# Performance work log

Hardware: AMD Instinct MI355X
Metric: run time of the kernel (lower is better)

The kernel has to match this reference:

```python
import jax, jax.numpy as jnp
import numpy as np

NEG_INF = -1e30  # stand-in for float('-inf') that is softmax-safe


def setup_inputs() -> dict:
    key = jax.random.key(0)
    ks = jax.random.split(key, 6)
    B, H, S, D = 2, 8, 1024, 64
    NF, K = 4, 3
    return {
        "query": jax.random.normal(ks[0], (B, H, S, D), dtype=jnp.float32),
        "keys": jax.random.normal(ks[1], (B, H, S, D), dtype=jnp.float32),
        "vals": jax.random.normal(ks[2], (B, H, S, D), dtype=jnp.float32),
        "mask": jnp.ones((B, 1, S, S), dtype=jnp.int32),
        "conv_w": jax.random.normal(ks[3], (NF, 1, K, K), dtype=jnp.float32) * (1.0 / K),
        "conv_b": jnp.zeros((NF,), dtype=jnp.float32),
        "lin_w": jax.random.normal(ks[4], (1, NF), dtype=jnp.float32) * 0.5,
        "lin_b": jnp.zeros((1,), dtype=jnp.float32),
    }


def reference(query, keys, vals, mask, conv_w, conv_b, lin_w, lin_b):
    B, H, S, D = query.shape
    NF = conv_w.shape[0]
    K = conv_w.shape[2]
    scale = jnp.asarray(D, query.dtype) ** 0.5

    # [B,H,S,S] raw dot-product scores
    dp = jnp.einsum("bhsd,bhtd->bhst", query, keys) / scale

    # conv2d over the score matrix: treat (B*H) as batch, 1 input channel
    x = dp.reshape(B * H, 1, S, S)
    conv = jax.lax.conv_general_dilated(
        x, conv_w,
        window_strides=(1, 1),
        padding=[(K // 2, K // 2), (K // 2, K // 2)],
        dimension_numbers=("NCHW", "OIHW", "NCHW"),
    ) + conv_b[None, :, None, None]
    conv = jax.nn.leaky_relu(conv, negative_slope=0.01)  # [B*H, NF, S, S]

    # per-pixel linear over the filter axis (Linear(num_filters, 1))
    conv = conv.reshape(B, H, NF, S, S)
    preattn = jnp.einsum("bhfst,f->bhst", conv, lin_w[0]) + lin_b[0]

    # masking + softmax (mask broadcasts over heads)
    preattn = jnp.where(mask == 0, jnp.asarray(NEG_INF, preattn.dtype), preattn)
    attn = jax.nn.softmax(preattn, axis=-1)

    # dropout is identity in eval mode
    return jnp.einsum("bhst,bhtd->bhsd", attn, vals)
```

## Files before the change

### kernel.cpp

```cpp
#include <hip/hip_runtime.h>
#include <math.h>

#define S_LEN 1024
#define D_DIM 64
#define NBH   16

typedef unsigned short ushort_t;
typedef unsigned int uint_t;
typedef __attribute__((ext_vector_type(8))) short short8;
typedef __attribute__((ext_vector_type(4))) short short4v;
typedef __attribute__((ext_vector_type(4))) float f32x4;
typedef __attribute__((ext_vector_type(2))) float f32x2;
typedef __attribute__((ext_vector_type(2))) _Float16 h2;

__device__ __forceinline__ ushort_t rne_bf16(float x) {
    unsigned u = __float_as_uint(x);
    return (ushort_t)((u + 0x7FFFu + ((u >> 16) & 1u)) >> 16);
}
__device__ __forceinline__ void split1(float x, ushort_t& h, ushort_t& l) {
    h = rne_bf16(x);
    float hf = __uint_as_float((unsigned)h << 16);
    l = rne_bf16(x - hf);
}
__device__ __forceinline__ ushort_t f16bits(float x) {
    _Float16 h = (_Float16)x;
    ushort_t b;
    __builtin_memcpy(&b, &h, 2);
    return b;
}
__device__ __forceinline__ float h2f(ushort_t b) {
    _Float16 h;
    __builtin_memcpy(&h, &b, 2);
    return (float)h;
}
__device__ __forceinline__ h2 as_h2(uint_t u) {
    h2 r;
    __builtin_memcpy(&r, &u, 4);
    return r;
}

__global__ __launch_bounds__(256) void prep(
    const float* __restrict__ k, const float* __restrict__ v,
    const int* __restrict__ mask,
    ushort_t* __restrict__ khi, ushort_t* __restrict__ klo,
    ushort_t* __restrict__ vhi, ushort_t* __restrict__ vlo,
    unsigned* __restrict__ mw)
{
    __shared__ float Ls[64][65];
    const int tid = threadIdx.x;
    const int bx = blockIdx.x;
    if (bx < 512) {
        const int gid  = bx * 256 + tid;
        const int bh   = gid >> 13;
        const int tile = (gid >> 7) & 63;
        const int ch   = (gid >> 6) & 1;
        const int lane = gid & 63;
        const int quad = lane >> 4, t15 = lane & 15;
        const float* src = k + ((size_t)bh * S_LEN + tile * 16 + t15) * D_DIM
                             + ch * 32 + quad * 8;
        float x[8];
        *(float4*)(x + 0) = *(const float4*)(src);
        *(float4*)(x + 4) = *(const float4*)(src + 4);
        short8 hv, lv;
        #pragma unroll
        for (int i = 0; i < 8; ++i) {
            ushort_t h, l;
            split1(x[i], h, l);
            hv[i] = (short)h; lv[i] = (short)l;
        }
        *(short8*)(khi + (size_t)gid * 8) = hv;
        *(short8*)(klo + (size_t)gid * 8) = lv;
    } else if (bx < 768) {
        const int bi = bx - 512;
        const int tt = bi & 15, bh = bi >> 4;
        const float* vb = v + ((size_t)bh * S_LEN + tt * 64) * D_DIM;
        #pragma unroll
        for (int p = 0; p < 4; ++p) {
            int idx = p * 1024 + tid * 4;
            int r = idx >> 6, c = idx & 63;
            float4 x = *(const float4*)(vb + r * 64 + c);
            Ls[r][c] = x.x; Ls[r][c+1] = x.y; Ls[r][c+2] = x.z; Ls[r][c+3] = x.w;
        }
        __syncthreads();
        const int d = tid >> 2, c0 = (tid & 3) * 16;
        ushort_t hi[16], lo[16];
        #pragma unroll
        for (int j = 0; j < 16; ++j) split1(Ls[c0 + j][d], hi[j], lo[j]);
        const int tb0 = tt * 8 + (c0 >> 3);
        const size_t o0 = (((size_t)bh * 128 + tb0) * 64 + d) * 8;
        const size_t o1 = (((size_t)bh * 128 + tb0 + 1) * 64 + d) * 8;
        *(short8*)(vhi + o0) = *(short8*)(hi);
        *(short8*)(vhi + o1) = *(short8*)(hi + 8);
        *(short8*)(vlo + o0) = *(short8*)(lo);
        *(short8*)(vlo + o1) = *(short8*)(lo + 8);
    } else {
        const int gid = (bx - 768) * 256 + tid;
        const int row = gid >> 5, wd = gid & 31;
        const int4* mp = (const int4*)(mask + (size_t)row * 1024 + wd * 32);
        unsigned bits = 0;
        #pragma unroll
        for (int p = 0; p < 8; ++p) {
            int4 qv = mp[p];
            bits |= (qv.x != 0 ? 1u : 0u) << (p * 4 + 0);
            bits |= (qv.y != 0 ? 1u : 0u) << (p * 4 + 1);
            bits |= (qv.z != 0 ? 1u : 0u) << (p * 4 + 2);
            bits |= (qv.w != 0 ? 1u : 0u) << (p * 4 + 3);
        }
        mw[(size_t)row * 32 + wd] = bits;
    }
}

#define DPSTR 1040
#define PSTR  1048
__global__ __launch_bounds__(512) void fused_qk_conv_av(
    const float* __restrict__ q,
    const ushort_t* __restrict__ khi, const ushort_t* __restrict__ klo,
    const unsigned* __restrict__ mw,
    const ushort_t* __restrict__ vhi, const ushort_t* __restrict__ vlo,
    const float* __restrict__ conv_w, const float* __restrict__ conv_b,
    const float* __restrict__ lin_w, const float* __restrict__ lin_b,
    float* __restrict__ out)
{
    __shared__ ushort_t dpH[18 * DPSTR];
    __shared__ ushort_t pP[16 * PSTR];
    __shared__ float oBuf[16][68];
    __shared__ float lsPart[16][4];
    __shared__ unsigned mb[16][32];

    const int st = blockIdx.x, bh = blockIdx.y;
    const int s0 = st * 16;
    const int b  = bh >> 3;
    const int tid = threadIdx.x;
    const int wave = tid >> 6, lane = tid & 63;
    const int m = lane & 15, quad = lane >> 4;

    {
        const int row = tid >> 5, wd = tid & 31;
        mb[row][wd] = mw[((size_t)b * S_LEN + s0 + row) * 32 + wd];
    }

    short8 AH0[2], AH1[2], AL0[2], AL1[2];
    #pragma unroll
    for (int set = 0; set < 2; ++set) {
        const int sA = s0 - 1 + 2 * set + m;
        const int sQ = sA < 0 ? 0 : (sA > S_LEN - 1 ? S_LEN - 1 : sA);
        const float* qp = q + ((size_t)bh * S_LEN + sQ) * D_DIM + quad * 8;
        float qa[16];
        *(float4*)(qa + 0)  = *(const float4*)(qp + 0);
        *(float4*)(qa + 4)  = *(const float4*)(qp + 4);
        *(float4*)(qa + 8)  = *(const float4*)(qp + 32);
        *(float4*)(qa + 12) = *(const float4*)(qp + 36);
        #pragma unroll
        for (int i = 0; i < 8; ++i) {
            ushort_t h, l;
            split1(qa[i] * 0.125f, h, l);
            AH0[set][i] = (short)h; AL0[set][i] = (short)l;
            split1(qa[8 + i] * 0.125f, h, l);
            AH1[set][i] = (short)h; AL1[set][i] = (short)l;
        }
    }

    #pragma unroll
    for (int tt = 0; tt < 8; ++tt) {
        const int tile = wave * 8 + tt;
        const size_t kb = (((size_t)bh * 64 + tile) * 128 + lane) * 8;
        short8 KH0 = *(const short8*)(khi + kb);
        short8 KL0 = *(const short8*)(klo + kb);
        short8 KH1 = *(const short8*)(khi + kb + 512);
        short8 KL1 = *(const short8*)(klo + kb + 512);
        const int col = tile * 16 + m;
        {
            f32x4 a0 = {0.f, 0.f, 0.f, 0.f}, a1 = {0.f, 0.f, 0.f, 0.f};
            a0 = __builtin_amdgcn_mfma_f32_16x16x32_bf16(AH0[0], KH0, a0, 0, 0, 0);
            a1 = __builtin_amdgcn_mfma_f32_16x16x32_bf16(AH1[0], KH1, a1, 0, 0, 0);
            a0 = __builtin_amdgcn_mfma_f32_16x16x32_bf16(AH0[0], KL0, a0, 0, 0, 0);
            a1 = __builtin_amdgcn_mfma_f32_16x16x32_bf16(AH1[0], KL1, a1, 0, 0, 0);
            a0 = __builtin_amdgcn_mfma_f32_16x16x32_bf16(AL0[0], KH0, a0, 0, 0, 0);
            a1 = __builtin_amdgcn_mfma_f32_16x16x32_bf16(AL1[0], KH1, a1, 0, 0, 0);
            #pragma unroll
            for (int r = 0; r < 4; ++r) {
                const int row = quad * 4 + r;
                const int s = s0 - 1 + row;
                const float v = (s >= 0 && s < S_LEN) ? a0[r] + a1[r] : 0.f;
                dpH[row * DPSTR + col] = f16bits(v);
            }
        }
        {
            f32x4 a0 = {0.f, 0.f, 0.f, 0.f}, a1 = {0.f, 0.f, 0.f, 0.f};
            a0 = __builtin_amdgcn_mfma_f32_16x16x32_bf16(AH0[1], KH0, a0, 0, 0, 0);
            a1 = __builtin_amdgcn_mfma_f32_16x16x32_bf16(AH1[1], KH1, a1, 0, 0, 0);
            a0 = __builtin_amdgcn_mfma_f32_16x16x32_bf16(AH0[1], KL0, a0, 0, 0, 0);
            a1 = __builtin_amdgcn_mfma_f32_16x16x32_bf16(AH1[1], KL1, a1, 0, 0, 0);
            a0 = __builtin_amdgcn_mfma_f32_16x16x32_bf16(AL0[1], KH0, a0, 0, 0, 0);
            a1 = __builtin_amdgcn_mfma_f32_16x16x32_bf16(AL1[1], KH1, a1, 0, 0, 0);
            if (quad == 3) {
                #pragma unroll
                for (int r = 2; r < 4; ++r) {
                    const int mrow = quad * 4 + r;
                    const int s = s0 + 1 + mrow;
                    const float v = (s < S_LEN) ? a0[r] + a1[r] : 0.f;
                    dpH[(mrow + 2) * DPSTR + col] = f16bits(v);
                }
            }
        }
    }

    float w[36];
    #pragma unroll
    for (int i = 0; i < 36; ++i) w[i] = conv_w[i];
    float cb[4], lw[4];
    #pragma unroll
    for (int f = 0; f < 4; ++f) { cb[f] = conv_b[f]; lw[f] = lin_w[f]; }
    const float lb = lin_b[0];

    __syncthreads();

    const int rh = tid >> 8, cg = tid & 255, c0 = cg * 4;
    #pragma unroll
    for (int pass = 0; pass < 2; ++pass) {
        const int obase = rh * 8 + pass * 4;
        float rowv[6][6];
        #pragma unroll
        for (int jj = 0; jj < 6; ++jj) {
            const ushort_t* rp = &dpH[(obase + jj) * DPSTR + c0];
            uint2 dd = *(const uint2*)rp;
            h2 p0 = as_h2(dd.x), p1 = as_h2(dd.y);
            rowv[jj][0] = cg ? h2f(rp[-1]) : 0.f;
            rowv[jj][1] = (float)p0[0]; rowv[jj][2] = (float)p0[1];
            rowv[jj][3] = (float)p1[0]; rowv[jj][4] = (float)p1[1];
            rowv[jj][5] = (cg < 255) ? h2f(rp[4]) : 0.f;
        }
        float ls[4];
        #pragma unroll
        for (int jo = 0; jo < 4; ++jo) {
            const int o = obase + jo;
            f32x2 pa = {lb, lb}, pb = {lb, lb};
            #pragma unroll
            for (int f = 0; f < 4; ++f) {
                f32x2 ca = {cb[f], cb[f]}, cbv = ca;
                #pragma unroll
                for (int dr = 0; dr < 3; ++dr) {
                    const float* vv = rowv[jo + dr];
                    #pragma unroll
                    for (int dc = 0; dc < 3; ++dc) {
                        const float wt = w[f * 9 + dr * 3 + dc];
                        f32x2 ia = {vv[dc],     vv[dc + 1]};
                        f32x2 ib = {vv[dc + 2], vv[dc + 3]};
                        ca  += wt * ia;
                        cbv += wt * ib;
                    }
                }
                f32x2 la  = {fmaxf(ca.x, 0.f)  + 0.01f * fminf(ca.x, 0.f),
                             fmaxf(ca.y, 0.f)  + 0.01f * fminf(ca.y, 0.f)};
                f32x2 lb2 = {fmaxf(cbv.x, 0.f) + 0.01f * fminf(cbv.x, 0.f),
                             fmaxf(cbv.y, 0.f) + 0.01f * fminf(cbv.y, 0.f)};
                pa += lw[f] * la;
                pb += lw[f] * lb2;
            }
            const unsigned word = mb[o][cg >> 3];
            const unsigned nib  = (word >> ((cg & 7) * 4)) & 0xFu;
            float pre[4] = {pa.x, pa.y, pb.x, pb.y};
            #pragma unroll
            for (int i = 0; i < 4; ++i)
                if (!((nib >> i) & 1u)) pre[i] = -1e30f;
            float pv[4];
            #pragma unroll
            for (int i = 0; i < 4; ++i) pv[i] = __expf(pre[i]);
            ls[jo] = (pv[0] + pv[1]) + (pv[2] + pv[3]);
            short4v hv = {(short)rne_bf16(pv[0]), (short)rne_bf16(pv[1]),
                          (short)rne_bf16(pv[2]), (short)rne_bf16(pv[3])};
            *(short4v*)&pP[o * PSTR + c0] = hv;
        }
        #pragma unroll
        for (int jo = 0; jo < 4; ++jo) {
            float t = ls[jo];
            #pragma unroll
            for (int off = 1; off < 64; off <<= 1) t += __shfl_xor(t, off);
            if (lane == 0) lsPart[obase + jo][wave & 3] = t;
        }
    }
    __syncthreads();

    const int d0 = (wave & 3) * 16;
    const int th = wave >> 2;
    f32x4 O = {0.f, 0.f, 0.f, 0.f};
    #pragma unroll 4
    for (int i = 0; i < 16; ++i) {
        const int c = th * 16 + i;
        short8 ph = *(const short8*)&pP[m * PSTR + c * 32 + quad * 8];
        const size_t vb = (((size_t)bh * 128 + c * 4 + quad) * 64 + d0 + m) * 8;
        short8 vh = *(const short8*)(vhi + vb);
        short8 vl = *(const short8*)(vlo + vb);
        O = __builtin_amdgcn_mfma_f32_16x16x32_bf16(ph, vh, O, 0, 0, 0);
        O = __builtin_amdgcn_mfma_f32_16x16x32_bf16(ph, vl, O, 0, 0, 0);
    }
    if (wave < 4) {
        #pragma unroll
        for (int r = 0; r < 4; ++r) oBuf[quad * 4 + r][d0 + m] = O[r];
    }
    __syncthreads();
    if (wave >= 4) {
        #pragma unroll
        for (int r = 0; r < 4; ++r) {
            const int br = quad * 4 + r;
            const float lsum = (lsPart[br][0] + lsPart[br][1]) +
                               (lsPart[br][2] + lsPart[br][3]);
            out[((size_t)bh * S_LEN + s0 + br) * D_DIM + d0 + m] =
                (O[r] + oBuf[br][d0 + m]) / lsum;
        }
    }
}

extern "C" void kernel_launch(void* const* d_in, const int* in_sizes, int n_in,
                              void* d_out, int out_size, void* d_ws, size_t ws_size,
                              hipStream_t stream) {
    const float* q      = (const float*)d_in[0];
    const float* k      = (const float*)d_in[1];
    const float* v      = (const float*)d_in[2];
    const int*   mask   = (const int*)d_in[3];
    const float* conv_w = (const float*)d_in[4];
    const float* conv_b = (const float*)d_in[5];
    const float* lin_w  = (const float*)d_in[6];
    const float* lin_b  = (const float*)d_in[7];
    float* out = (float*)d_out;

    char* wsb = (char*)d_ws;
    const size_t MB = 1024 * 1024;
    ushort_t* khi = (ushort_t*)(wsb + 0 * MB);
    ushort_t* klo = (ushort_t*)(wsb + 2 * MB);
    ushort_t* vhi = (ushort_t*)(wsb + 4 * MB);
    ushort_t* vlo = (ushort_t*)(wsb + 6 * MB);
    unsigned* mw  = (unsigned*)(wsb + 8 * MB);

    prep<<<dim3(1024), 256, 0, stream>>>(k, v, mask, khi, klo, vhi, vlo, mw);
    fused_qk_conv_av<<<dim3(64, NBH), 512, 0, stream>>>(
        q, khi, klo, mw, vhi, vlo, conv_w, conv_b, lin_w, lin_b, out);
}
```

Measured before the change: 131.8 us.

## Compute halo rows inside 16-row tile and emit 14 output rows per block

Each block now computes 16 score rows that include its own conv halo and writes only the 14 interior rows, so the second MFMA set used for the two extra halo rows is removed. The grid grows to 74 row-blocks per head to cover the sequence, and inactive rows skip the conv and softmax work. The conv and leaky-relu math is also rewritten with explicit vector FMA/min/max builtins. The cost is more blocks and redundant AV work on halo rows.

```diff
diff --git a/kernel.cpp b/kernel.cpp
--- a/kernel.cpp
+++ b/kernel.cpp
@@ -4,6 +4,8 @@
 #define S_LEN 1024
 #define D_DIM 64
 #define NBH   16
+#define RPB   14
+#define NSB   74
 
 typedef unsigned short ushort_t;
 typedef unsigned int uint_t;
@@ -121,43 +123,40 @@
     const float* __restrict__ lin_w, const float* __restrict__ lin_b,
     float* __restrict__ out)
 {
-    __shared__ ushort_t dpH[18 * DPSTR];
+    __shared__ ushort_t dpH[16 * DPSTR];
     __shared__ ushort_t pP[16 * PSTR];
     __shared__ float oBuf[16][68];
     __shared__ float lsPart[16][4];
     __shared__ unsigned mb[16][32];
 
     const int st = blockIdx.x, bh = blockIdx.y;
-    const int s0 = st * 16;
+    const int s0 = st * RPB;
     const int b  = bh >> 3;
     const int tid = threadIdx.x;
     const int wave = tid >> 6, lane = tid & 63;
     const int m = lane & 15, quad = lane >> 4;
 
     {
-        const int row = tid >> 5, wd = tid & 31;
-        mb[row][wd] = mw[((size_t)b * S_LEN + s0 + row) * 32 + wd];
-    }
-
-    short8 AH0[2], AH1[2], AL0[2], AL1[2];
-    #pragma unroll
-    for (int set = 0; set < 2; ++set) {
-        const int sA = s0 - 1 + 2 * set + m;
-        const int sQ = sA < 0 ? 0 : (sA > S_LEN - 1 ? S_LEN - 1 : sA);
-        const float* qp = q + ((size_t)bh * S_LEN + sQ) * D_DIM + quad * 8;
-        float qa[16];
-        *(float4*)(qa + 0)  = *(const float4*)(qp + 0);
-        *(float4*)(qa + 4)  = *(const float4*)(qp + 4);
-        *(float4*)(qa + 8)  = *(const float4*)(qp + 32);
-        *(float4*)(qa + 12) = *(const float4*)(qp + 36);
-        #pragma unroll
-        for (int i = 0; i < 8; ++i) {
-            ushort_t h, l;
-            split1(qa[i] * 0.125f, h, l);
-            AH0[set][i] = (short)h; AL0[set][i] = (short)l;
-            split1(qa[8 + i] * 0.125f, h, l);
-            AH1[set][i] = (short)h; AL1[set][i] = (short)l;
-        }
+        const int o = tid >> 5, wd = tid & 31;
+        const int s = s0 - 1 + o;
+        mb[o][wd] = (s >= 0 && s < S_LEN)
+                  ? mw[((size_t)b * S_LEN + s) * 32 + wd] : 0u;
+    }
+
+    const int sA = s0 - 1 + m;
+    const int sQ = sA < 0 ? 0 : (sA > S_LEN - 1 ? S_LEN - 1 : sA);
+    const float* qp = q + ((size_t)bh * S_LEN + sQ) * D_DIM + quad * 8;
+    float qa[16];
+    *(float4*)(qa + 0)  = *(const float4*)(qp + 0);
+    *(float4*)(qa + 4)  = *(const float4*)(qp + 4);
+    *(float4*)(qa + 8)  = *(const float4*)(qp + 32);
+    *(float4*)(qa + 12) = *(const float4*)(qp + 36);
+    short8 AH0, AH1, AL0, AL1;
+    #pragma unroll
+    for (int i = 0; i < 8; ++i) {
+        ushort_t h, l;
+        split1(qa[i] * 0.125f, h, l);      AH0[i] = (short)h; AL0[i] = (short)l;
+        split1(qa[8 + i] * 0.125f, h, l);  AH1[i] = (short)h; AL1[i] = (short)l;
     }
 
     #pragma unroll
@@ -168,40 +167,20 @@
         short8 KL0 = *(const short8*)(klo + kb);
         short8 KH1 = *(const short8*)(khi + kb + 512);
         short8 KL1 = *(const short8*)(klo + kb + 512);
+        f32x4 a0 = {0.f, 0.f, 0.f, 0.f}, a1 = {0.f, 0.f, 0.f, 0.f};
+        a0 = __builtin_amdgcn_mfma_f32_16x16x32_bf16(AH0, KH0, a0, 0, 0, 0);
+        a1 = __builtin_amdgcn_mfma_f32_16x16x32_bf16(AH1, KH1, a1, 0, 0, 0);
+        a0 = __builtin_amdgcn_mfma_f32_16x16x32_bf16(AH0, KL0, a0, 0, 0, 0);
+        a1 = __builtin_amdgcn_mfma_f32_16x16x32_bf16(AH1, KL1, a1, 0, 0, 0);
+        a0 = __builtin_amdgcn_mfma_f32_16x16x32_bf16(AL0, KH0, a0, 0, 0, 0);
+        a1 = __builtin_amdgcn_mfma_f32_16x16x32_bf16(AL1, KH1, a1, 0, 0, 0);
         const int col = tile * 16 + m;
-        {
-            f32x4 a0 = {0.f, 0.f, 0.f, 0.f}, a1 = {0.f, 0.f, 0.f, 0.f};
-            a0 = __builtin_amdgcn_mfma_f32_16x16x32_bf16(AH0[0], KH0, a0, 0, 0, 0);
-            a1 = __builtin_amdgcn_mfma_f32_16x16x32_bf16(AH1[0], KH1, a1, 0, 0, 0);
-            a0 = __builtin_amdgcn_mfma_f32_16x16x32_bf16(AH0[0], KL0, a0, 0, 0, 0);
-            a1 = __builtin_amdgcn_mfma_f32_16x16x32_bf16(AH1[0], KL1, a1, 0, 0, 0);
-            a0 = __builtin_amdgcn_mfma_f32_16x16x32_bf16(AL0[0], KH0, a0, 0, 0, 0);
-            a1 = __builtin_amdgcn_mfma_f32_16x16x32_bf16(AL1[0], KH1, a1, 0, 0, 0);
-            #pragma unroll
-            for (int r = 0; r < 4; ++r) {
-                const int row = quad * 4 + r;
-                const int s = s0 - 1 + row;
-                const float v = (s >= 0 && s < S_LEN) ? a0[r] + a1[r] : 0.f;
-                dpH[row * DPSTR + col] = f16bits(v);
-            }
-        }
-        {
-            f32x4 a0 = {0.f, 0.f, 0.f, 0.f}, a1 = {0.f, 0.f, 0.f, 0.f};
-            a0 = __builtin_amdgcn_mfma_f32_16x16x32_bf16(AH0[1], KH0, a0, 0, 0, 0);
-            a1 = __builtin_amdgcn_mfma_f32_16x16x32_bf16(AH1[1], KH1, a1, 0, 0, 0);
-            a0 = __builtin_amdgcn_mfma_f32_16x16x32_bf16(AH0[1], KL0, a0, 0, 0, 0);
-            a1 = __builtin_amdgcn_mfma_f32_16x16x32_bf16(AH1[1], KL1, a1, 0, 0, 0);
-            a0 = __builtin_amdgcn_mfma_f32_16x16x32_bf16(AL0[1], KH0, a0, 0, 0, 0);
-            a1 = __builtin_amdgcn_mfma_f32_16x16x32_bf16(AL1[1], KH1, a1, 0, 0, 0);
-            if (quad == 3) {
-                #pragma unroll
-                for (int r = 2; r < 4; ++r) {
-                    const int mrow = quad * 4 + r;
-                    const int s = s0 + 1 + mrow;
-                    const float v = (s < S_LEN) ? a0[r] + a1[r] : 0.f;
-                    dpH[(mrow + 2) * DPSTR + col] = f16bits(v);
-                }
-            }
+        #pragma unroll
+        for (int r = 0; r < 4; ++r) {
+            const int row = quad * 4 + r;
+            const int s = s0 - 1 + row;
+            const float v = (s >= 0 && s < S_LEN) ? a0[r] + a1[r] : 0.f;
+            dpH[row * DPSTR + col] = f16bits(v);
         }
     }
 
@@ -212,6 +191,8 @@
     #pragma unroll
     for (int f = 0; f < 4; ++f) { cb[f] = conv_b[f]; lw[f] = lin_w[f]; }
     const float lb = lin_b[0];
+    const f32x2 zero2 = {0.f, 0.f};
+    const f32x2 c001  = {0.01f, 0.01f};
 
     __syncthreads();
 
@@ -222,54 +203,71 @@
         float rowv[6][6];
         #pragma unroll
         for (int jj = 0; jj < 6; ++jj) {
-            const ushort_t* rp = &dpH[(obase + jj) * DPSTR + c0];
-            uint2 dd = *(const uint2*)rp;
-            h2 p0 = as_h2(dd.x), p1 = as_h2(dd.y);
-            rowv[jj][0] = cg ? h2f(rp[-1]) : 0.f;
-            rowv[jj][1] = (float)p0[0]; rowv[jj][2] = (float)p0[1];
-            rowv[jj][3] = (float)p1[0]; rowv[jj][4] = (float)p1[1];
-            rowv[jj][5] = (cg < 255) ? h2f(rp[4]) : 0.f;
+            const int dr = obase - 1 + jj;
+            if (dr >= 0 && dr < 16) {
+                const ushort_t* rp = &dpH[dr * DPSTR + c0];
+                uint2 dd = *(const uint2*)rp;
+                h2 p0 = as_h2(dd.x), p1 = as_h2(dd.y);
+                rowv[jj][0] = cg ? h2f(rp[-1]) : 0.f;
+                rowv[jj][1] = (float)p0[0]; rowv[jj][2] = (float)p0[1];
+                rowv[jj][3] = (float)p1[0]; rowv[jj][4] = (float)p1[1];
+                rowv[jj][5] = (cg < 255) ? h2f(rp[4]) : 0.f;
+            } else {
+                #pragma unroll
+                for (int i = 0; i < 6; ++i) rowv[jj][i] = 0.f;
+            }
         }
         float ls[4];
         #pragma unroll
         for (int jo = 0; jo < 4; ++jo) {
             const int o = obase + jo;
-            f32x2 pa = {lb, lb}, pb = {lb, lb};
-            #pragma unroll
-            for (int f = 0; f < 4; ++f) {
-                f32x2 ca = {cb[f], cb[f]}, cbv = ca;
+            const bool act = (o >= 1) && (o <= RPB) && (s0 - 1 + o < S_LEN);
+            if (act) {
+                f32x2 pa = {lb, lb}, pb = {lb, lb};
                 #pragma unroll
-                for (int dr = 0; dr < 3; ++dr) {
-                    const float* vv = rowv[jo + dr];
+                for (int f = 0; f < 4; ++f) {
+                    f32x2 ca = {cb[f], cb[f]}, cbv = ca;
                     #pragma unroll
-                    for (int dc = 0; dc < 3; ++dc) {
-                        const float wt = w[f * 9 + dr * 3 + dc];
-                        f32x2 ia = {vv[dc],     vv[dc + 1]};
-                        f32x2 ib = {vv[dc + 2], vv[dc + 3]};
-                        ca  += wt * ia;
-                        cbv += wt * ib;
+                    for (int dr = 0; dr < 3; ++dr) {
+                        const float* vv = rowv[jo + dr];
+                        #pragma unroll
+                        for (int dc = 0; dc < 3; ++dc) {
+                            const float wt = w[f * 9 + dr * 3 + dc];
+                            const f32x2 wt2 = {wt, wt};
+                            f32x2 ia = {vv[dc],     vv[dc + 1]};
+                            f32x2 ib = {vv[dc + 2], vv[dc + 3]};
+                            ca  = __builtin_elementwise_fma(wt2, ia, ca);
+                            cbv = __builtin_elementwise_fma(wt2, ib, cbv);
+                        }
                     }
+                    const f32x2 lwv = {lw[f], lw[f]};
+                    f32x2 la  = __builtin_elementwise_fma(
+                        c001, __builtin_elementwise_min(ca, zero2),
+                        __builtin_elementwise_max(ca, zero2));
+                    f32x2 lb2 = __builtin_elementwise_fma(
+                        c001, __builtin_elementwise_min(cbv, zero2),
+                        __builtin_elementwise_max(cbv, zero2));
+                    pa = __builtin_elementwise_fma(lwv, la, pa);
+                    pb = __builtin_elementwise_fma(lwv, lb2, pb);
                 }
-                f32x2 la  = {fmaxf(ca.x, 0.f)  + 0.01f * fminf(ca.x, 0.f),
-                             fmaxf(ca.y, 0.f)  + 0.01f * fminf(ca.y, 0.f)};
-                f32x2 lb2 = {fmaxf(cbv.x, 0.f) + 0.01f * fminf(cbv.x, 0.f),
-                             fmaxf(cbv.y, 0.f) + 0.01f * fminf(cbv.y, 0.f)};
-                pa += lw[f] * la;
-                pb += lw[f] * lb2;
+                const unsigned word = mb[o][cg >> 3];
+                const unsigned nib  = (word >> ((cg & 7) * 4)) & 0xFu;
+                float pre[4] = {pa.x, pa.y, pb.x, pb.y};
+                #pragma unroll
+                for (int i = 0; i < 4; ++i)
+                    if (!((nib >> i) & 1u)) pre[i] = -1e30f;
+                float pv[4];
+                #pragma unroll
+                for (int i = 0; i < 4; ++i) pv[i] = __expf(pre[i]);
+                ls[jo] = (pv[0] + pv[1]) + (pv[2] + pv[3]);
+                short4v hv = {(short)rne_bf16(pv[0]), (short)rne_bf16(pv[1]),
+                              (short)rne_bf16(pv[2]), (short)rne_bf16(pv[3])};
+                *(short4v*)&pP[o * PSTR + c0] = hv;
+            } else {
+                short4v z = {0, 0, 0, 0};
+                *(short4v*)&pP[o * PSTR + c0] = z;
+                ls[jo] = 0.f;
             }
-            const unsigned word = mb[o][cg >> 3];
-            const unsigned nib  = (word >> ((cg & 7) * 4)) & 0xFu;
-            float pre[4] = {pa.x, pa.y, pb.x, pb.y};
-            #pragma unroll
-            for (int i = 0; i < 4; ++i)
-                if (!((nib >> i) & 1u)) pre[i] = -1e30f;
-            float pv[4];
-            #pragma unroll
-            for (int i = 0; i < 4; ++i) pv[i] = __expf(pre[i]);
-            ls[jo] = (pv[0] + pv[1]) + (pv[2] + pv[3]);
-            short4v hv = {(short)rne_bf16(pv[0]), (short)rne_bf16(pv[1]),
-                          (short)rne_bf16(pv[2]), (short)rne_bf16(pv[3])};
-            *(short4v*)&pP[o * PSTR + c0] = hv;
         }
         #pragma unroll
         for (int jo = 0; jo < 4; ++jo) {
@@ -303,10 +301,13 @@
         #pragma unroll
         for (int r = 0; r < 4; ++r) {
             const int br = quad * 4 + r;
-            const float lsum = (lsPart[br][0] + lsPart[br][1]) +
-                               (lsPart[br][2] + lsPart[br][3]);
-            out[((size_t)bh * S_LEN + s0 + br) * D_DIM + d0 + m] =
-                (O[r] + oBuf[br][d0 + m]) / lsum;
+            const int s = s0 - 1 + br;
+            if (br >= 1 && br <= RPB && s < S_LEN) {
+                const float lsum = (lsPart[br][0] + lsPart[br][1]) +
+                                   (lsPart[br][2] + lsPart[br][3]);
+                out[((size_t)bh * S_LEN + s) * D_DIM + d0 + m] =
+                    (O[r] + oBuf[br][d0 + m]) / lsum;
+            }
         }
     }
 }
@@ -333,6 +334,6 @@
     unsigned* mw  = (unsigned*)(wsb + 8 * MB);
 
     prep<<<dim3(1024), 256, 0, stream>>>(k, v, mask, khi, klo, vhi, vlo, mw);
-    fused_qk_conv_av<<<dim3(64, NBH), 512, 0, stream>>>(
+    fused_qk_conv_av<<<dim3(NSB, NBH), 512, 0, stream>>>(
         q, khi, klo, mw, vhi, vlo, conv_w, conv_b, lin_w, lin_b, out);
 }
```

Result: no change. 131.4 us (-0.3%).
